# Kernel tuning notes

Measured on AMD Instinct MI355X. Metric: run time of the kernel, lower is better.

## Reference

```python
import jax, jax.numpy as jnp
import numpy as np

B, H, L, D = 16, 8, 128, 64
SCALE = jnp.float32(np.sqrt(D))
NEG = jnp.float32(-1e9)


def setup_inputs() -> dict:
    key = jax.random.key(0)
    kq, kk, kv, km = jax.random.split(key, 4)
    Q = jax.random.normal(kq, (B, H, L, D), dtype=jnp.float32)
    K = jax.random.normal(kk, (H, B, L, D), dtype=jnp.float32)
    V = jax.random.normal(kv, (H, B, L, D), dtype=jnp.float32)
    mask = jax.random.randint(km, (B, 1, 1, L, L), 0, 2, dtype=jnp.int32)
    return {"Q": Q, "K": K, "V": V, "mask": mask}


def reference(Q, K, V, mask):
    # Cross-sample (intersample) attention:
    # scores[b,h,c,i,j] = <Q[b,h,i,:], K[h,c,j,:]> / sqrt(D)  -> (B,H,B,L,L)
    scores = jnp.einsum('bhid,hcjd->bhcij', Q, K) / SCALE
    scores = jnp.where(mask == 0, NEG, scores)
    attn_weights = jax.nn.softmax(scores, axis=-1)  # (B,H,B,L,L)
    # output[b,h,c,i,:] = sum_j w[b,h,c,i,j] * V[h,c,j,:]  -> (B,H,B,L,D)
    output = jnp.einsum('bhcij,hcjd->bhcid', attn_weights, V)
    return (output, attn_weights)
```

## Files before the change

### kernel.cpp

```cpp
#include <hip/hip_runtime.h>
#include <hip/hip_bf16.h>

typedef float  f32x4  __attribute__((ext_vector_type(4)));
typedef __bf16 bf16x8 __attribute__((ext_vector_type(8)));

#define MFMA16(A,B,C) __builtin_amdgcn_mfma_f32_16x16x32_bf16((A),(B),(C),0,0,0)

constexpr int BN = 16, HN = 8, LN = 128, DN = 64;
constexpr size_t OUT0 = (size_t)BN * HN * BN * LN * DN;

constexpr int QE = BN * HN * LN * DN;
constexpr size_t WS_BYTES = (size_t)4 * QE * sizeof(__bf16);

constexpr int PS  = 36;
constexpr int KTS = 72;
constexpr int VTS = 136;


__device__ __forceinline__ void load8_split(const float* __restrict__ p, float scale,
                                            bf16x8& hi, bf16x8& lo) {
  float f[8];
  *(float4*)&f[0] = *(const float4*)(p);
  *(float4*)&f[4] = *(const float4*)(p + 4);
#pragma unroll
  for (int i = 0; i < 8; ++i) {
    float x = f[i] * scale;
    __bf16 h = (__bf16)x;
    hi[i] = h;
    lo[i] = (__bf16)(x - (float)h);
  }
}

__device__ __forceinline__ void lds8_split(const float* p, bf16x8& hi, bf16x8& lo) {
  float f[8];
  *(float4*)&f[0] = *(const float4*)(p);
  *(float4*)&f[4] = *(const float4*)(p + 4);
#pragma unroll
  for (int i = 0; i < 8; ++i) {
    __bf16 h = (__bf16)f[i];
    hi[i] = h;
    lo[i] = (__bf16)(f[i] - (float)h);
  }
}

__device__ __forceinline__ void gload_lds16(const void* g, void* l) {
  __builtin_amdgcn_global_load_lds(
      (const __attribute__((address_space(1))) unsigned int*)g,
      (__attribute__((address_space(3))) unsigned int*)l, 16, 0, 0);
}

__global__ __launch_bounds__(256) void pre_kernel(
    const float* __restrict__ Q, const float* __restrict__ K,
    const float* __restrict__ V, __bf16* __restrict__ ws)
{
  const int t   = threadIdx.x;
  const int blk = blockIdx.x;

  if (blk < 512) {
    int base = blk * 2048 + t * 8;
    float f[8];
    *(float4*)&f[0] = *(const float4*)(Q + base);
    *(float4*)&f[4] = *(const float4*)(Q + base + 4);
    bf16x8 hi, lo;
#pragma unroll
    for (int i = 0; i < 8; ++i) {
      float x = f[i] * 0.125f;
      __bf16 h = (__bf16)x;
      hi[i] = h;
      lo[i] = (__bf16)(x - (float)h);
    }
    *(bf16x8*)&ws[base]      = hi;
    *(bf16x8*)&ws[QE + base] = lo;
  } else if (blk < 1024) {
    int g  = (blk - 512) * 256 + t;
    int k0 = (g & 7) * 8;
    int n  = (g >> 3) & 127;
    int hc = g >> 10;
    const float* src = K + ((size_t)hc * LN + n) * DN + k0;
    float f[8];
    *(float4*)&f[0] = *(const float4*)(src);
    *(float4*)&f[4] = *(const float4*)(src + 4);
    bf16x8 kk;
#pragma unroll
    for (int i = 0; i < 8; ++i) kk[i] = (__bf16)f[i];
    int k0s = k0 ^ ((n & 7) << 3);
    *(bf16x8*)&ws[2 * (size_t)QE + (size_t)hc * 8192 + n * 64 + k0s] = kk;
  } else {
    int hc = blk - 1024;
    int j8 = t >> 4;
    int d0 = (t & 15) * 4;
    const float* Vp = V + (size_t)hc * (LN * DN);
    float4 vv[8];
#pragma unroll
    for (int r = 0; r < 8; ++r)
      vv[r] = *(const float4*)(Vp + (j8 * 8 + r) * DN + d0);
#pragma unroll
    for (int dw = 0; dw < 4; ++dw) {
      int d = d0 + dw;
      bf16x8 col;
#pragma unroll
      for (int r = 0; r < 8; ++r)
        col[r] = (__bf16)(((const float*)&vv[r])[dw]);
      int js = (j8 * 8) ^ ((d & 7) << 3);
      *(bf16x8*)&ws[3 * (size_t)QE + (size_t)hc * 8192 + d * 128 + js] = col;
    }
  }
}

__global__ __launch_bounds__(256, 3) void isa_attn_fast(
    const __bf16* __restrict__ ws, const int* __restrict__ M,
    float* __restrict__ out)
{
  __shared__ __bf16 KT[LN * DN];
  __shared__ __bf16 VT[DN * LN];
  __shared__ float  P [LN * PS];

  const int bid = blockIdx.x;
  const int w = (bid & 7) * 256 + (bid >> 3);
  const int h = w >> 8;
  const int c = (w >> 4) & 15;
  const int b = w & 15;
  const int hc = h * BN + c;

  const __bf16* Qh = ws + (size_t)(b * HN + h) * (LN * DN);
  const __bf16* Ql = Qh + QE;
  const __bf16* Ks = ws + 2 * (size_t)QE + (size_t)hc * 8192;
  const __bf16* Vs = ws + 3 * (size_t)QE + (size_t)hc * 8192;
  const int*   Mp = M + (size_t)b * (LN * LN);
  float* Op = out + (size_t)((b * HN + h) * BN + c) * (LN * DN);
  float* Wp = out + OUT0 + (size_t)((b * HN + h) * BN + c) * (LN * LN);

  const int t    = threadIdx.x;
  const int lane = t & 63;
  const int wid  = t >> 6;
  const int quad = lane >> 4;
  const int l16  = lane & 15;
  const int row0 = wid * 32;
  const int swz  = (l16 & 7) << 3;

  {
    const char* kg = (const char*)Ks;
    const char* vg = (const char*)Vs;
    char* kl = (char*)KT;
    char* vl = (char*)VT;
#pragma unroll
    for (int i = 0; i < 4; ++i)
      gload_lds16(kg + t * 16 + i * 4096, kl + t * 16 + i * 4096);
#pragma unroll
    for (int i = 0; i < 4; ++i)
      gload_lds16(vg + t * 16 + i * 4096, vl + t * 16 + i * 4096);
  }

  bf16x8 qhi[2][2], qlo[2][2];
#pragma unroll
  for (int rt = 0; rt < 2; ++rt)
#pragma unroll
    for (int kt = 0; kt < 2; ++kt) {
      const int off = (row0 + rt * 16 + l16) * DN + kt * 32 + quad * 8;
      qhi[rt][kt] = *(const bf16x8*)(Qh + off);
      qlo[rt][kt] = *(const bf16x8*)(Ql + off);
    }

  __syncthreads();

  f32x4 acc[2][8];
#pragma unroll
  for (int rt = 0; rt < 2; ++rt)
#pragma unroll
    for (int ct = 0; ct < 8; ++ct)
      acc[rt][ct] = (f32x4){0.f, 0.f, 0.f, 0.f};

#pragma unroll
  for (int ct = 0; ct < 8; ++ct) {
#pragma unroll
    for (int kt = 0; kt < 2; ++kt) {
      bf16x8 kh = *(const bf16x8*)&KT[(ct * 16 + l16) * 64 + ((kt * 32 + quad * 8) ^ swz)];
#pragma unroll
      for (int rt = 0; rt < 2; ++rt) {
        acc[rt][ct] = MFMA16(qhi[rt][kt], kh, acc[rt][ct]);
        acc[rt][ct] = MFMA16(qlo[rt][kt], kh, acc[rt][ct]);
      }
    }
  }

#pragma unroll
  for (int rt = 0; rt < 2; ++rt) {
#pragma unroll
    for (int r = 0; r < 4; ++r) {
      int row = row0 + rt * 16 + quad * 4 + r;
      const int* mrow = Mp + (size_t)row * LN + l16;
      float mf[8];
#pragma unroll
      for (int ct = 0; ct < 8; ++ct) mf[ct] = (float)mrow[ct * 16];
      float mx = -3.0e38f;
#pragma unroll
      for (int ct = 0; ct < 8; ++ct) mx = fmaxf(mx, acc[rt][ct][r]);
      mx = fmaxf(mx, __shfl_xor(mx, 1));
      mx = fmaxf(mx, __shfl_xor(mx, 2));
      mx = fmaxf(mx, __shfl_xor(mx, 4));
      mx = fmaxf(mx, __shfl_xor(mx, 8));
      float s[8];
      float sum = 0.f;
#pragma unroll
      for (int ct = 0; ct < 8; ++ct) {
        s[ct] = __expf(acc[rt][ct][r] - mx) * mf[ct];
        sum += s[ct];
      }
      sum += __shfl_xor(sum, 1);
      sum += __shfl_xor(sum, 2);
      sum += __shfl_xor(sum, 4);
      sum += __shfl_xor(sum, 8);
      float inv = __builtin_amdgcn_rcpf(sum);
      inv = inv * (2.0f - sum * inv);
#pragma unroll
      for (int ct = 0; ct < 8; ++ct) acc[rt][ct][r] = s[ct] * inv;
    }
  }

  f32x4 oacc[2][4];
#pragma unroll
  for (int rt = 0; rt < 2; ++rt)
#pragma unroll
    for (int nt = 0; nt < 4; ++nt)
      oacc[rt][nt] = (f32x4){0.f, 0.f, 0.f, 0.f};

#pragma unroll
  for (int qu = 0; qu < 4; ++qu) {
#pragma unroll
    for (int rt = 0; rt < 2; ++rt)
#pragma unroll
      for (int cc = 0; cc < 2; ++cc)
#pragma unroll
        for (int r = 0; r < 4; ++r)
          P[(row0 + rt * 16 + quad * 4 + r) * PS + cc * 16 + l16] =
              acc[rt][qu * 2 + cc][r];

#pragma unroll
    for (int e = 0; e < 4; ++e) {
      int idx = e * 64 + lane;
      int rl  = idx >> 3;
      int c4  = idx & 7;
      float4 v = *(const float4*)&P[(row0 + rl) * PS + c4 * 4];
      *(float4*)&Wp[(size_t)(row0 + rl) * LN + qu * 32 + c4 * 4] = v;
    }

    bf16x8 phi[2], plo[2];
#pragma unroll
    for (int rt = 0; rt < 2; ++rt)
      lds8_split(&P[(row0 + rt * 16 + l16) * PS + quad * 8], phi[rt], plo[rt]);
#pragma unroll
    for (int nt = 0; nt < 4; ++nt) {
      bf16x8 vh = *(const bf16x8*)&VT[(nt * 16 + l16) * 128 + ((qu * 32 + quad * 8) ^ swz)];
#pragma unroll
      for (int rt = 0; rt < 2; ++rt) {
        oacc[rt][nt] = MFMA16(phi[rt], vh, oacc[rt][nt]);
        oacc[rt][nt] = MFMA16(plo[rt], vh, oacc[rt][nt]);
      }
    }
  }

#pragma unroll
  for (int hf = 0; hf < 2; ++hf) {
#pragma unroll
    for (int rt = 0; rt < 2; ++rt)
#pragma unroll
      for (int nn = 0; nn < 2; ++nn)
#pragma unroll
        for (int r = 0; r < 4; ++r)
          P[(row0 + rt * 16 + quad * 4 + r) * PS + nn * 16 + l16] =
              oacc[rt][hf * 2 + nn][r];
#pragma unroll
    for (int e = 0; e < 4; ++e) {
      int idx = e * 64 + lane;
      int rl  = idx >> 3;
      int c4  = idx & 7;
      float4 v = *(const float4*)&P[(row0 + rl) * PS + c4 * 4];
      *(float4*)&Op[(size_t)(row0 + rl) * DN + hf * 32 + c4 * 4] = v;
    }
  }
}

__global__ __launch_bounds__(256, 3) void isa_attn_kernel(
    const float* __restrict__ Q, const float* __restrict__ K,
    const float* __restrict__ V, const int* __restrict__ M,
    float* __restrict__ out)
{
  __shared__ __bf16 KT[LN * KTS];
  __shared__ __bf16 VT[DN * VTS];
  __shared__ float  P [LN * PS];

  const int bid = blockIdx.x;
  const int w = (bid & 7) * 256 + (bid >> 3);
  const int h = w >> 8;
  const int c = (w >> 4) & 15;
  const int b = w & 15;

  const float* Qp = Q + (size_t)(b * HN + h) * (LN * DN);
  const float* Kp = K + (size_t)(h * BN + c) * (LN * DN);
  const float* Vp = V + (size_t)(h * BN + c) * (LN * DN);
  const int*   Mp = M + (size_t)b * (LN * LN);
  float* Op = out + (size_t)((b * HN + h) * BN + c) * (LN * DN);
  float* Wp = out + OUT0 + (size_t)((b * HN + h) * BN + c) * (LN * LN);

  const int t    = threadIdx.x;
  const int lane = t & 63;
  const int wid  = t >> 6;
  const int quad = lane >> 4;
  const int l16  = lane & 15;
  const int row0 = wid * 32;

#pragma unroll
  for (int it = 0; it < 4; ++it) {
    int idx = t + it * 256;
    int n  = idx >> 3;
    int k0 = (idx & 7) * 8;
    float4 a0 = *(const float4*)(Kp + n * DN + k0);
    float4 a1 = *(const float4*)(Kp + n * DN + k0 + 4);
    bf16x8 kk;
    kk[0] = (__bf16)a0.x; kk[1] = (__bf16)a0.y; kk[2] = (__bf16)a0.z; kk[3] = (__bf16)a0.w;
    kk[4] = (__bf16)a1.x; kk[5] = (__bf16)a1.y; kk[6] = (__bf16)a1.z; kk[7] = (__bf16)a1.w;
    *(bf16x8*)&KT[n * KTS + k0] = kk;
  }

  {
    int j8 = t >> 4;
    int d0 = (t & 15) * 4;
    float4 vv[8];
#pragma unroll
    for (int r = 0; r < 8; ++r)
      vv[r] = *(const float4*)(Vp + (j8 * 8 + r) * DN + d0);
#pragma unroll
    for (int dw = 0; dw < 4; ++dw) {
      bf16x8 col;
#pragma unroll
      for (int r = 0; r < 8; ++r)
        col[r] = (__bf16)(((const float*)&vv[r])[dw]);
      *(bf16x8*)&VT[(d0 + dw) * VTS + j8 * 8] = col;
    }
  }

  bf16x8 qhi[2][2], qlo[2][2];
#pragma unroll
  for (int rt = 0; rt < 2; ++rt)
#pragma unroll
    for (int kt = 0; kt < 2; ++kt)
      load8_split(Qp + (row0 + rt * 16 + l16) * DN + kt * 32 + quad * 8, 0.125f,
                  qhi[rt][kt], qlo[rt][kt]);

  __syncthreads();

  f32x4 acc[2][8];
#pragma unroll
  for (int rt = 0; rt < 2; ++rt)
#pragma unroll
    for (int ct = 0; ct < 8; ++ct)
      acc[rt][ct] = (f32x4){0.f, 0.f, 0.f, 0.f};

#pragma unroll
  for (int ct = 0; ct < 8; ++ct) {
#pragma unroll
    for (int kt = 0; kt < 2; ++kt) {
      bf16x8 kh = *(const bf16x8*)&KT[(ct * 16 + l16) * KTS + kt * 32 + quad * 8];
#pragma unroll
      for (int rt = 0; rt < 2; ++rt) {
        acc[rt][ct] = MFMA16(qhi[rt][kt], kh, acc[rt][ct]);
        acc[rt][ct] = MFMA16(qlo[rt][kt], kh, acc[rt][ct]);
      }
    }
  }

#pragma unroll
  for (int rt = 0; rt < 2; ++rt) {
#pragma unroll
    for (int r = 0; r < 4; ++r) {
      int row = row0 + rt * 16 + quad * 4 + r;
      const int* mrow = Mp + (size_t)row * LN + l16;
      float mf[8];
#pragma unroll
      for (int ct = 0; ct < 8; ++ct) mf[ct] = (float)mrow[ct * 16];
      float mx = -3.0e38f;
#pragma unroll
      for (int ct = 0; ct < 8; ++ct) mx = fmaxf(mx, acc[rt][ct][r]);
      mx = fmaxf(mx, __shfl_xor(mx, 1));
      mx = fmaxf(mx, __shfl_xor(mx, 2));
      mx = fmaxf(mx, __shfl_xor(mx, 4));
      mx = fmaxf(mx, __shfl_xor(mx, 8));
      float s[8];
      float sum = 0.f;
#pragma unroll
      for (int ct = 0; ct < 8; ++ct) {
        s[ct] = __expf(acc[rt][ct][r] - mx) * mf[ct];
        sum += s[ct];
      }
      sum += __shfl_xor(sum, 1);
      sum += __shfl_xor(sum, 2);
      sum += __shfl_xor(sum, 4);
      sum += __shfl_xor(sum, 8);
      float inv = __builtin_amdgcn_rcpf(sum);
      inv = inv * (2.0f - sum * inv);
#pragma unroll
      for (int ct = 0; ct < 8; ++ct) acc[rt][ct][r] = s[ct] * inv;
    }
  }

  f32x4 oacc[2][4];
#pragma unroll
  for (int rt = 0; rt < 2; ++rt)
#pragma unroll
    for (int nt = 0; nt < 4; ++nt)
      oacc[rt][nt] = (f32x4){0.f, 0.f, 0.f, 0.f};

#pragma unroll
  for (int qu = 0; qu < 4; ++qu) {
#pragma unroll
    for (int rt = 0; rt < 2; ++rt)
#pragma unroll
      for (int cc = 0; cc < 2; ++cc)
#pragma unroll
        for (int r = 0; r < 4; ++r)
          P[(row0 + rt * 16 + quad * 4 + r) * PS + cc * 16 + l16] =
              acc[rt][qu * 2 + cc][r];

#pragma unroll
    for (int e = 0; e < 4; ++e) {
      int idx = e * 64 + lane;
      int rl  = idx >> 3;
      int c4  = idx & 7;
      float4 v = *(const float4*)&P[(row0 + rl) * PS + c4 * 4];
      *(float4*)&Wp[(size_t)(row0 + rl) * LN + qu * 32 + c4 * 4] = v;
    }

    bf16x8 phi[2], plo[2];
#pragma unroll
    for (int rt = 0; rt < 2; ++rt)
      lds8_split(&P[(row0 + rt * 16 + l16) * PS + quad * 8], phi[rt], plo[rt]);
#pragma unroll
    for (int nt = 0; nt < 4; ++nt) {
      bf16x8 vh = *(const bf16x8*)&VT[(nt * 16 + l16) * VTS + qu * 32 + quad * 8];
#pragma unroll
      for (int rt = 0; rt < 2; ++rt) {
        oacc[rt][nt] = MFMA16(phi[rt], vh, oacc[rt][nt]);
        oacc[rt][nt] = MFMA16(plo[rt], vh, oacc[rt][nt]);
      }
    }
  }

#pragma unroll
  for (int hf = 0; hf < 2; ++hf) {
#pragma unroll
    for (int rt = 0; rt < 2; ++rt)
#pragma unroll
      for (int nn = 0; nn < 2; ++nn)
#pragma unroll
        for (int r = 0; r < 4; ++r)
          P[(row0 + rt * 16 + quad * 4 + r) * PS + nn * 16 + l16] =
              oacc[rt][hf * 2 + nn][r];
#pragma unroll
    for (int e = 0; e < 4; ++e) {
      int idx = e * 64 + lane;
      int rl  = idx >> 3;
      int c4  = idx & 7;
      float4 v = *(const float4*)&P[(row0 + rl) * PS + c4 * 4];
      *(float4*)&Op[(size_t)(row0 + rl) * DN + hf * 32 + c4 * 4] = v;
    }
  }
}

extern "C" void kernel_launch(void* const* d_in, const int* in_sizes, int n_in,
                              void* d_out, int out_size, void* d_ws, size_t ws_size,
                              hipStream_t stream) {
  const float* Q = (const float*)d_in[0];
  const float* K = (const float*)d_in[1];
  const float* V = (const float*)d_in[2];
  const int*   M = (const int*)d_in[3];
  if (d_ws != nullptr && ws_size >= WS_BYTES) {
    __bf16* ws = (__bf16*)d_ws;
    pre_kernel<<<dim3(1152), dim3(256), 0, stream>>>(Q, K, V, ws);
    isa_attn_fast<<<dim3(BN * HN * BN), dim3(256), 0, stream>>>(ws, M, (float*)d_out);
  } else {
    isa_attn_kernel<<<dim3(BN * HN * BN), dim3(256), 0, stream>>>(Q, K, V, M, (float*)d_out);
  }
}
```

Baseline: 222.5 us.

## Pre-convert mask to bf16 in lane-friendly layout and use nontemporal loads/stores

Result: slower. 228.2 us (+2.6%).

```diff
diff --git a/kernel.cpp b/kernel.cpp
--- a/kernel.cpp
+++ b/kernel.cpp
@@ -10,7 +10,8 @@
 constexpr size_t OUT0 = (size_t)BN * HN * BN * LN * DN;
 
 constexpr int QE = BN * HN * LN * DN;
-constexpr size_t WS_BYTES = (size_t)4 * QE * sizeof(__bf16);
+constexpr size_t MBOFF = 4 * (size_t)QE;
+constexpr size_t WS_BYTES = (MBOFF + (size_t)BN * LN * LN) * sizeof(__bf16);
 
 constexpr int PS  = 36;
 constexpr int KTS = 72;
@@ -49,9 +50,17 @@
       (__attribute__((address_space(3))) unsigned int*)l, 16, 0, 0);
 }
 
+__device__ __forceinline__ f32x4 ntld4(const float* p) {
+  return __builtin_nontemporal_load((const f32x4*)p);
+}
+__device__ __forceinline__ void ntst4(float* p, f32x4 v) {
+  __builtin_nontemporal_store(v, (f32x4*)p);
+}
+
 __global__ __launch_bounds__(256) void pre_kernel(
     const float* __restrict__ Q, const float* __restrict__ K,
-    const float* __restrict__ V, __bf16* __restrict__ ws)
+    const float* __restrict__ V, const int* __restrict__ M,
+    __bf16* __restrict__ ws)
 {
   const int t   = threadIdx.x;
   const int blk = blockIdx.x;
@@ -59,8 +68,8 @@
   if (blk < 512) {
     int base = blk * 2048 + t * 8;
     float f[8];
-    *(float4*)&f[0] = *(const float4*)(Q + base);
-    *(float4*)&f[4] = *(const float4*)(Q + base + 4);
+    *(f32x4*)&f[0] = ntld4(Q + base);
+    *(f32x4*)&f[4] = ntld4(Q + base + 4);
     bf16x8 hi, lo;
 #pragma unroll
     for (int i = 0; i < 8; ++i) {
@@ -78,38 +87,52 @@
     int hc = g >> 10;
     const float* src = K + ((size_t)hc * LN + n) * DN + k0;
     float f[8];
-    *(float4*)&f[0] = *(const float4*)(src);
-    *(float4*)&f[4] = *(const float4*)(src + 4);
+    *(f32x4*)&f[0] = ntld4(src);
+    *(f32x4*)&f[4] = ntld4(src + 4);
     bf16x8 kk;
 #pragma unroll
     for (int i = 0; i < 8; ++i) kk[i] = (__bf16)f[i];
     int k0s = k0 ^ ((n & 7) << 3);
     *(bf16x8*)&ws[2 * (size_t)QE + (size_t)hc * 8192 + n * 64 + k0s] = kk;
-  } else {
+  } else if (blk < 1152) {
     int hc = blk - 1024;
     int j8 = t >> 4;
     int d0 = (t & 15) * 4;
     const float* Vp = V + (size_t)hc * (LN * DN);
-    float4 vv[8];
+    f32x4 vv[8];
 #pragma unroll
     for (int r = 0; r < 8; ++r)
-      vv[r] = *(const float4*)(Vp + (j8 * 8 + r) * DN + d0);
+      vv[r] = ntld4(Vp + (j8 * 8 + r) * DN + d0);
 #pragma unroll
     for (int dw = 0; dw < 4; ++dw) {
       int d = d0 + dw;
       bf16x8 col;
 #pragma unroll
       for (int r = 0; r < 8; ++r)
-        col[r] = (__bf16)(((const float*)&vv[r])[dw]);
+        col[r] = (__bf16)vv[r][dw];
       int js = (j8 * 8) ^ ((d & 7) << 3);
       *(bf16x8*)&ws[3 * (size_t)QE + (size_t)hc * 8192 + d * 128 + js] = col;
     }
+  } else {
+    int bsel = blk - 1152;
+    const int* src = M + (size_t)bsel * (LN * LN);
+    __bf16*    dst = ws + MBOFF + (size_t)bsel * (LN * LN);
+    int row  = t >> 1;
+    int half = t & 1;
+#pragma unroll
+    for (int g = 0; g < 8; ++g) {
+      int l16 = half * 8 + g;
+      bf16x8 m8;
+#pragma unroll
+      for (int ct = 0; ct < 8; ++ct)
+        m8[ct] = (__bf16)(float)src[row * LN + ct * 16 + l16];
+      *(bf16x8*)&dst[row * LN + l16 * 8] = m8;
+    }
   }
 }
 
 __global__ __launch_bounds__(256, 3) void isa_attn_fast(
-    const __bf16* __restrict__ ws, const int* __restrict__ M,
-    float* __restrict__ out)
+    const __bf16* __restrict__ ws, float* __restrict__ out)
 {
   __shared__ __bf16 KT[LN * DN];
   __shared__ __bf16 VT[DN * LN];
@@ -126,7 +149,7 @@
   const __bf16* Ql = Qh + QE;
   const __bf16* Ks = ws + 2 * (size_t)QE + (size_t)hc * 8192;
   const __bf16* Vs = ws + 3 * (size_t)QE + (size_t)hc * 8192;
-  const int*   Mp = M + (size_t)b * (LN * LN);
+  const __bf16* Mb = ws + MBOFF + (size_t)b * (LN * LN);
   float* Op = out + (size_t)((b * HN + h) * BN + c) * (LN * DN);
   float* Wp = out + OUT0 + (size_t)((b * HN + h) * BN + c) * (LN * LN);
 
@@ -175,6 +198,193 @@
 #pragma unroll
     for (int kt = 0; kt < 2; ++kt) {
       bf16x8 kh = *(const bf16x8*)&KT[(ct * 16 + l16) * 64 + ((kt * 32 + quad * 8) ^ swz)];
+#pragma unroll
+      for (int rt = 0; rt < 2; ++rt) {
+        acc[rt][ct] = MFMA16(qhi[rt][kt], kh, acc[rt][ct]);
+        acc[rt][ct] = MFMA16(qlo[rt][kt], kh, acc[rt][ct]);
+      }
+    }
+  }
+
+#pragma unroll
+  for (int rt = 0; rt < 2; ++rt) {
+    bf16x8 m8[4];
+#pragma unroll
+    for (int r = 0; r < 4; ++r) {
+      int row = row0 + rt * 16 + quad * 4 + r;
+      m8[r] = *(const bf16x8*)&Mb[row * LN + l16 * 8];
+    }
+#pragma unroll
+    for (int r = 0; r < 4; ++r) {
+      float mx = -3.0e38f;
+#pragma unroll
+      for (int ct = 0; ct < 8; ++ct) mx = fmaxf(mx, acc[rt][ct][r]);
+      mx = fmaxf(mx, __shfl_xor(mx, 1));
+      mx = fmaxf(mx, __shfl_xor(mx, 2));
+      mx = fmaxf(mx, __shfl_xor(mx, 4));
+      mx = fmaxf(mx, __shfl_xor(mx, 8));
+      float s[8];
+      float sum = 0.f;
+#pragma unroll
+      for (int ct = 0; ct < 8; ++ct) {
+        s[ct] = __expf(acc[rt][ct][r] - mx) * (float)m8[r][ct];
+        sum += s[ct];
+      }
+      sum += __shfl_xor(sum, 1);
+      sum += __shfl_xor(sum, 2);
+      sum += __shfl_xor(sum, 4);
+      sum += __shfl_xor(sum, 8);
+      float inv = __builtin_amdgcn_rcpf(sum);
+      inv = inv * (2.0f - sum * inv);
+#pragma unroll
+      for (int ct = 0; ct < 8; ++ct) acc[rt][ct][r] = s[ct] * inv;
+    }
+  }
+
+  f32x4 oacc[2][4];
+#pragma unroll
+  for (int rt = 0; rt < 2; ++rt)
+#pragma unroll
+    for (int nt = 0; nt < 4; ++nt)
+      oacc[rt][nt] = (f32x4){0.f, 0.f, 0.f, 0.f};
+
+#pragma unroll
+  for (int qu = 0; qu < 4; ++qu) {
+#pragma unroll
+    for (int rt = 0; rt < 2; ++rt)
+#pragma unroll
+      for (int cc = 0; cc < 2; ++cc)
+#pragma unroll
+        for (int r = 0; r < 4; ++r)
+          P[(row0 + rt * 16 + quad * 4 + r) * PS + cc * 16 + l16] =
+              acc[rt][qu * 2 + cc][r];
+
+#pragma unroll
+    for (int e = 0; e < 4; ++e) {
+      int idx = e * 64 + lane;
+      int rl  = idx >> 3;
+      int c4  = idx & 7;
+      f32x4 v = *(const f32x4*)&P[(row0 + rl) * PS + c4 * 4];
+      ntst4(&Wp[(size_t)(row0 + rl) * LN + qu * 32 + c4 * 4], v);
+    }
+
+    bf16x8 phi[2], plo[2];
+#pragma unroll
+    for (int rt = 0; rt < 2; ++rt)
+      lds8_split(&P[(row0 + rt * 16 + l16) * PS + quad * 8], phi[rt], plo[rt]);
+#pragma unroll
+    for (int nt = 0; nt < 4; ++nt) {
+      bf16x8 vh = *(const bf16x8*)&VT[(nt * 16 + l16) * 128 + ((qu * 32 + quad * 8) ^ swz)];
+#pragma unroll
+      for (int rt = 0; rt < 2; ++rt) {
+        oacc[rt][nt] = MFMA16(phi[rt], vh, oacc[rt][nt]);
+        oacc[rt][nt] = MFMA16(plo[rt], vh, oacc[rt][nt]);
+      }
+    }
+  }
+
+#pragma unroll
+  for (int hf = 0; hf < 2; ++hf) {
+#pragma unroll
+    for (int rt = 0; rt < 2; ++rt)
+#pragma unroll
+      for (int nn = 0; nn < 2; ++nn)
+#pragma unroll
+        for (int r = 0; r < 4; ++r)
+          P[(row0 + rt * 16 + quad * 4 + r) * PS + nn * 16 + l16] =
+              oacc[rt][hf * 2 + nn][r];
+#pragma unroll
+    for (int e = 0; e < 4; ++e) {
+      int idx = e * 64 + lane;
+      int rl  = idx >> 3;
+      int c4  = idx & 7;
+      f32x4 v = *(const f32x4*)&P[(row0 + rl) * PS + c4 * 4];
+      ntst4(&Op[(size_t)(row0 + rl) * DN + hf * 32 + c4 * 4], v);
+    }
+  }
+}
+
+__global__ __launch_bounds__(256, 3) void isa_attn_kernel(
+    const float* __restrict__ Q, const float* __restrict__ K,
+    const float* __restrict__ V, const int* __restrict__ M,
+    float* __restrict__ out)
+{
+  __shared__ __bf16 KT[LN * KTS];
+  __shared__ __bf16 VT[DN * VTS];
+  __shared__ float  P [LN * PS];
+
+  const int bid = blockIdx.x;
+  const int w = (bid & 7) * 256 + (bid >> 3);
+  const int h = w >> 8;
+  const int c = (w >> 4) & 15;
+  const int b = w & 15;
+
+  const float* Qp = Q + (size_t)(b * HN + h) * (LN * DN);
+  const float* Kp = K + (size_t)(h * BN + c) * (LN * DN);
+  const float* Vp = V + (size_t)(h * BN + c) * (LN * DN);
+  const int*   Mp = M + (size_t)b * (LN * LN);
+  float* Op = out + (size_t)((b * HN + h) * BN + c) * (LN * DN);
+  float* Wp = out + OUT0 + (size_t)((b * HN + h) * BN + c) * (LN * LN);
+
+  const int t    = threadIdx.x;
+  const int lane = t & 63;
+  const int wid  = t >> 6;
+  const int quad = lane >> 4;
+  const int l16  = lane & 15;
+  const int row0 = wid * 32;
+
+#pragma unroll
+  for (int it = 0; it < 4; ++it) {
+    int idx = t + it * 256;
+    int n  = idx >> 3;
+    int k0 = (idx & 7) * 8;
+    float4 a0 = *(const float4*)(Kp + n * DN + k0);
+    float4 a1 = *(const float4*)(Kp + n * DN + k0 + 4);
+    bf16x8 kk;
+    kk[0] = (__bf16)a0.x; kk[1] = (__bf16)a0.y; kk[2] = (__bf16)a0.z; kk[3] = (__bf16)a0.w;
+    kk[4] = (__bf16)a1.x; kk[5] = (__bf16)a1.y; kk[6] = (__bf16)a1.z; kk[7] = (__bf16)a1.w;
+    *(bf16x8*)&KT[n * KTS + k0] = kk;
+  }
+
+  {
+    int j8 = t >> 4;
+    int d0 = (t & 15) * 4;
+    float4 vv[8];
+#pragma unroll
+    for (int r = 0; r < 8; ++r)
+      vv[r] = *(const float4*)(Vp + (j8 * 8 + r) * DN + d0);
+#pragma unroll
+    for (int dw = 0; dw < 4; ++dw) {
+      bf16x8 col;
+#pragma unroll
+      for (int r = 0; r < 8; ++r)
+        col[r] = (__bf16)(((const float*)&vv[r])[dw]);
+      *(bf16x8*)&VT[(d0 + dw) * VTS + j8 * 8] = col;
+    }
+  }
+
+  bf16x8 qhi[2][2], qlo[2][2];
+#pragma unroll
+  for (int rt = 0; rt < 2; ++rt)
+#pragma unroll
+    for (int kt = 0; kt < 2; ++kt)
+      load8_split(Qp + (row0 + rt * 16 + l16) * DN + kt * 32 + quad * 8, 0.125f,
+                  qhi[rt][kt], qlo[rt][kt]);
+
+  __syncthreads();
+
+  f32x4 acc[2][8];
+#pragma unroll
+  for (int rt = 0; rt < 2; ++rt)
+#pragma unroll
+    for (int ct = 0; ct < 8; ++ct)
+      acc[rt][ct] = (f32x4){0.f, 0.f, 0.f, 0.f};
+
+#pragma unroll
+  for (int ct = 0; ct < 8; ++ct) {
+#pragma unroll
+    for (int kt = 0; kt < 2; ++kt) {
+      bf16x8 kh = *(const bf16x8*)&KT[(ct * 16 + l16) * KTS + kt * 32 + quad * 8];
 #pragma unroll
       for (int rt = 0; rt < 2; ++rt) {
         acc[rt][ct] = MFMA16(qhi[rt][kt], kh, acc[rt][ct]);
@@ -250,192 +460,6 @@
       lds8_split(&P[(row0 + rt * 16 + l16) * PS + quad * 8], phi[rt], plo[rt]);
 #pragma unroll
     for (int nt = 0; nt < 4; ++nt) {
-      bf16x8 vh = *(const bf16x8*)&VT[(nt * 16 + l16) * 128 + ((qu * 32 + quad * 8) ^ swz)];
-#pragma unroll
-      for (int rt = 0; rt < 2; ++rt) {
-        oacc[rt][nt] = MFMA16(phi[rt], vh, oacc[rt][nt]);
-        oacc[rt][nt] = MFMA16(plo[rt], vh, oacc[rt][nt]);
-      }
-    }
-  }
-
-#pragma unroll
-  for (int hf = 0; hf < 2; ++hf) {
-#pragma unroll
-    for (int rt = 0; rt < 2; ++rt)
-#pragma unroll
-      for (int nn = 0; nn < 2; ++nn)
-#pragma unroll
-        for (int r = 0; r < 4; ++r)
-          P[(row0 + rt * 16 + quad * 4 + r) * PS + nn * 16 + l16] =
-              oacc[rt][hf * 2 + nn][r];
-#pragma unroll
-    for (int e = 0; e < 4; ++e) {
-      int idx = e * 64 + lane;
-      int rl  = idx >> 3;
-      int c4  = idx & 7;
-      float4 v = *(const float4*)&P[(row0 + rl) * PS + c4 * 4];
-      *(float4*)&Op[(size_t)(row0 + rl) * DN + hf * 32 + c4 * 4] = v;
-    }
-  }
-}
-
-__global__ __launch_bounds__(256, 3) void isa_attn_kernel(
-    const float* __restrict__ Q, const float* __restrict__ K,
-    const float* __restrict__ V, const int* __restrict__ M,
-    float* __restrict__ out)
-{
-  __shared__ __bf16 KT[LN * KTS];
-  __shared__ __bf16 VT[DN * VTS];
-  __shared__ float  P [LN * PS];
-
-  const int bid = blockIdx.x;
-  const int w = (bid & 7) * 256 + (bid >> 3);
-  const int h = w >> 8;
-  const int c = (w >> 4) & 15;
-  const int b = w & 15;
-
-  const float* Qp = Q + (size_t)(b * HN + h) * (LN * DN);
-  const float* Kp = K + (size_t)(h * BN + c) * (LN * DN);
-  const float* Vp = V + (size_t)(h * BN + c) * (LN * DN);
-  const int*   Mp = M + (size_t)b * (LN * LN);
-  float* Op = out + (size_t)((b * HN + h) * BN + c) * (LN * DN);
-  float* Wp = out + OUT0 + (size_t)((b * HN + h) * BN + c) * (LN * LN);
-
-  const int t    = threadIdx.x;
-  const int lane = t & 63;
-  const int wid  = t >> 6;
-  const int quad = lane >> 4;
-  const int l16  = lane & 15;
-  const int row0 = wid * 32;
-
-#pragma unroll
-  for (int it = 0; it < 4; ++it) {
-    int idx = t + it * 256;
-    int n  = idx >> 3;
-    int k0 = (idx & 7) * 8;
-    float4 a0 = *(const float4*)(Kp + n * DN + k0);
-    float4 a1 = *(const float4*)(Kp + n * DN + k0 + 4);
-    bf16x8 kk;
-    kk[0] = (__bf16)a0.x; kk[1] = (__bf16)a0.y; kk[2] = (__bf16)a0.z; kk[3] = (__bf16)a0.w;
-    kk[4] = (__bf16)a1.x; kk[5] = (__bf16)a1.y; kk[6] = (__bf16)a1.z; kk[7] = (__bf16)a1.w;
-    *(bf16x8*)&KT[n * KTS + k0] = kk;
-  }
-
-  {
-    int j8 = t >> 4;
-    int d0 = (t & 15) * 4;
-    float4 vv[8];
-#pragma unroll
-    for (int r = 0; r < 8; ++r)
-      vv[r] = *(const float4*)(Vp + (j8 * 8 + r) * DN + d0);
-#pragma unroll
-    for (int dw = 0; dw < 4; ++dw) {
-      bf16x8 col;
-#pragma unroll
-      for (int r = 0; r < 8; ++r)
-        col[r] = (__bf16)(((const float*)&vv[r])[dw]);
-      *(bf16x8*)&VT[(d0 + dw) * VTS + j8 * 8] = col;
-    }
-  }
-
-  bf16x8 qhi[2][2], qlo[2][2];
-#pragma unroll
-  for (int rt = 0; rt < 2; ++rt)
-#pragma unroll
-    for (int kt = 0; kt < 2; ++kt)
-      load8_split(Qp + (row0 + rt * 16 + l16) * DN + kt * 32 + quad * 8, 0.125f,
-                  qhi[rt][kt], qlo[rt][kt]);
-
-  __syncthreads();
-
-  f32x4 acc[2][8];
-#pragma unroll
-  for (int rt = 0; rt < 2; ++rt)
-#pragma unroll
-    for (int ct = 0; ct < 8; ++ct)
-      acc[rt][ct] = (f32x4){0.f, 0.f, 0.f, 0.f};
-
-#pragma unroll
-  for (int ct = 0; ct < 8; ++ct) {
-#pragma unroll
-    for (int kt = 0; kt < 2; ++kt) {
-      bf16x8 kh = *(const bf16x8*)&KT[(ct * 16 + l16) * KTS + kt * 32 + quad * 8];
-#pragma unroll
-      for (int rt = 0; rt < 2; ++rt) {
-        acc[rt][ct] = MFMA16(qhi[rt][kt], kh, acc[rt][ct]);
-        acc[rt][ct] = MFMA16(qlo[rt][kt], kh, acc[rt][ct]);
-      }
-    }
-  }
-
-#pragma unroll
-  for (int rt = 0; rt < 2; ++rt) {
-#pragma unroll
-    for (int r = 0; r < 4; ++r) {
-      int row = row0 + rt * 16 + quad * 4 + r;
-      const int* mrow = Mp + (size_t)row * LN + l16;
-      float mf[8];
-#pragma unroll
-      for (int ct = 0; ct < 8; ++ct) mf[ct] = (float)mrow[ct * 16];
-      float mx = -3.0e38f;
-#pragma unroll
-      for (int ct = 0; ct < 8; ++ct) mx = fmaxf(mx, acc[rt][ct][r]);
-      mx = fmaxf(mx, __shfl_xor(mx, 1));
-      mx = fmaxf(mx, __shfl_xor(mx, 2));
-      mx = fmaxf(mx, __shfl_xor(mx, 4));
-      mx = fmaxf(mx, __shfl_xor(mx, 8));
-      float s[8];
-      float sum = 0.f;
-#pragma unroll
-      for (int ct = 0; ct < 8; ++ct) {
-        s[ct] = __expf(acc[rt][ct][r] - mx) * mf[ct];
-        sum += s[ct];
-      }
-      sum += __shfl_xor(sum, 1);
-      sum += __shfl_xor(sum, 2);
-      sum += __shfl_xor(sum, 4);
-      sum += __shfl_xor(sum, 8);
-      float inv = __builtin_amdgcn_rcpf(sum);
-      inv = inv * (2.0f - sum * inv);
-#pragma unroll
-      for (int ct = 0; ct < 8; ++ct) acc[rt][ct][r] = s[ct] * inv;
-    }
-  }
-
-  f32x4 oacc[2][4];
-#pragma unroll
-  for (int rt = 0; rt < 2; ++rt)
-#pragma unroll
-    for (int nt = 0; nt < 4; ++nt)
-      oacc[rt][nt] = (f32x4){0.f, 0.f, 0.f, 0.f};
-
-#pragma unroll
-  for (int qu = 0; qu < 4; ++qu) {
-#pragma unroll
-    for (int rt = 0; rt < 2; ++rt)
-#pragma unroll
-      for (int cc = 0; cc < 2; ++cc)
-#pragma unroll
-        for (int r = 0; r < 4; ++r)
-          P[(row0 + rt * 16 + quad * 4 + r) * PS + cc * 16 + l16] =
-              acc[rt][qu * 2 + cc][r];
-
-#pragma unroll
-    for (int e = 0; e < 4; ++e) {
-      int idx = e * 64 + lane;
-      int rl  = idx >> 3;
-      int c4  = idx & 7;
-      float4 v = *(const float4*)&P[(row0 + rl) * PS + c4 * 4];
-      *(float4*)&Wp[(size_t)(row0 + rl) * LN + qu * 32 + c4 * 4] = v;
-    }
-
-    bf16x8 phi[2], plo[2];
-#pragma unroll
-    for (int rt = 0; rt < 2; ++rt)
-      lds8_split(&P[(row0 + rt * 16 + l16) * PS + quad * 8], phi[rt], plo[rt]);
-#pragma unroll
-    for (int nt = 0; nt < 4; ++nt) {
       bf16x8 vh = *(const bf16x8*)&VT[(nt * 16 + l16) * VTS + qu * 32 + quad * 8];
 #pragma unroll
       for (int rt = 0; rt < 2; ++rt) {
@@ -475,8 +499,8 @@
   const int*   M = (const int*)d_in[3];
   if (d_ws != nullptr && ws_size >= WS_BYTES) {
     __bf16* ws = (__bf16*)d_ws;
-    pre_kernel<<<dim3(1152), dim3(256), 0, stream>>>(Q, K, V, ws);
-    isa_attn_fast<<<dim3(BN * HN * BN), dim3(256), 0, stream>>>(ws, M, (float*)d_out);
+    pre_kernel<<<dim3(1168), dim3(256), 0, stream>>>(Q, K, V, M, ws);
+    isa_attn_fast<<<dim3(BN * HN * BN), dim3(256), 0, stream>>>(ws, (float*)d_out);
   } else {
     isa_attn_kernel<<<dim3(BN * HN * BN), dim3(256), 0, stream>>>(Q, K, V, M, (float*)d_out);
   }
```
